# Performance work log

Hardware: AMD Instinct MI355X
Metric: run time of the kernel (lower is better)

The kernel has to match this reference:

```python
import jax, jax.numpy as jnp
import numpy as np

H, C = 2, 32  # heads, out_channels per head
NEG_SLOPE = 0.2


def gatv2_layer(h, src, dst, ea, W, b, We, att, bias, N):
    # shared lin_l = lin_r (share_weights=True)
    z = (h @ W + b).reshape(N, H, C)                      # [N,H,C]
    e = (ea @ We).reshape(-1, H, C)                        # [E',H,C]
    s = jax.nn.leaky_relu(z[dst] + z[src] + e, NEG_SLOPE)  # [E',H,C]
    alpha = jnp.einsum('ehc,hc->eh', s, att)               # [E',H]
    # segment softmax over destination neighborhoods
    m = jax.ops.segment_max(alpha, dst, num_segments=N)
    m = jnp.where(jnp.isfinite(m), m, 0.0)
    ex = jnp.exp(alpha - m[dst])
    denom = jax.ops.segment_sum(ex, dst, num_segments=N)
    a = ex / (denom[dst] + 1e-16)                          # [E',H]
    msg = (z[src] * a[:, :, None]).reshape(-1, H * C)      # [E',H*C]
    out = jax.ops.segment_sum(msg, dst, num_segments=N) + bias
    return out                                             # [N,H*C]


def setup_inputs() -> dict:
    key = jax.random.key(0)
    ks = jax.random.split(key, 16)
    N, E = 50000, 800000
    inp = {
        'x': jax.random.normal(ks[0], (N, 2), jnp.float32),
        'edge_index': jax.random.randint(ks[1], (2, E), 0, N, jnp.int64 if jax.config.jax_enable_x64 else jnp.int32).astype(jnp.int32),
        'edge_attr': jax.random.uniform(ks[2], (E, 2), jnp.float32),
        'dest_index': 123,
        'W0': jax.random.normal(ks[3], (2, 64), jnp.float32) * 0.5,
        'b0': jnp.zeros((64,), jnp.float32),
        'We0': jax.random.normal(ks[4], (2, 64), jnp.float32) * 0.5,
        'att0': jax.random.normal(ks[5], (H, C), jnp.float32) * 0.5,
        'bias0': jnp.zeros((64,), jnp.float32),
        'W1': jax.random.normal(ks[6], (64, 64), jnp.float32) * 0.125,
        'b1': jnp.zeros((64,), jnp.float32),
        'We1': jax.random.normal(ks[7], (2, 64), jnp.float32) * 0.5,
        'att1': jax.random.normal(ks[8], (H, C), jnp.float32) * 0.5,
        'bias1': jnp.zeros((64,), jnp.float32),
        'Wm1': jax.random.normal(ks[9], (194, 32), jnp.float32) * 0.07,
        'bm1': jnp.zeros((32,), jnp.float32),
        'Wm2': jax.random.normal(ks[10], (32, 1), jnp.float32) * 0.17,
        'bm2': jnp.zeros((1,), jnp.float32),
    }
    return inp


def reference(x, edge_index, edge_attr, dest_index,
              W0, b0, We0, att0, bias0,
              W1, b1, We1, att1, bias1,
              Wm1, bm1, Wm2, bm2):
    N = x.shape[0]
    # add self loops (fill_value='mean' for edge_attr)
    loops = jnp.arange(N, dtype=edge_index.dtype)
    src = jnp.concatenate([edge_index[0], loops])
    dst = jnp.concatenate([edge_index[1], loops])
    ea_sl = jnp.concatenate(
        [edge_attr, jnp.broadcast_to(edge_attr.mean(axis=0), (N, edge_attr.shape[1]))], axis=0)

    h = x
    h = jax.nn.elu(gatv2_layer(h, src, dst, ea_sl, W0, b0, We0, att0, bias0, N))
    h = jax.nn.elu(gatv2_layer(h, src, dst, ea_sl, W1, b1, We1, att1, bias1, N))

    goal = h[dest_index]                                   # [64]
    src_emb = h[edge_index[0]]                             # [E,64]
    dst_emb = h[edge_index[1]]                             # [E,64]
    goal_rep = jnp.broadcast_to(goal, (edge_index.shape[1], goal.shape[0]))
    edge_in = jnp.concatenate([src_emb, dst_emb, goal_rep, edge_attr], axis=-1)  # [E,194]
    hmlp = jax.nn.relu(edge_in @ Wm1 + bm1)
    logits = (hmlp @ Wm2 + bm2).squeeze(-1)                # [E]
    return logits
```

## Files before the change

kernel.cpp:

```cpp
#include <hip/hip_runtime.h>
#include <hip/hip_bf16.h>
#include <hip/hip_fp16.h>
#include <math.h>


typedef __attribute__((ext_vector_type(8))) short short8;
typedef __attribute__((ext_vector_type(4))) float f32x4;

#define BSH 6
#define CAP 2048
#define CH 4096

template <int IMM>
__device__ __forceinline__ float swz(float x) {
    return __int_as_float(__builtin_amdgcn_ds_swizzle(__float_as_int(x), IMM));
}

template <int CTRL>
__device__ __forceinline__ float dpp_add(float p) {
    int t = __builtin_amdgcn_update_dpp(0, __float_as_int(p), CTRL, 0xF, 0xF, true);
    return p + __int_as_float(t);
}

__device__ __forceinline__ short2 bsplit(float x) {
    unsigned u = __float_as_uint(x);
    short hi = (short)(u >> 16);
    float hif = __uint_as_float(u & 0xFFFF0000u);
    short lo = (short)(__float_as_uint(x - hif) >> 16);
    return make_short2(hi, lo);
}

__global__ __launch_bounds__(512) void setup_kernel(const float* __restrict__ W1,
                                                    const float* __restrict__ Wm1,
                                                    short* __restrict__ BfW1,
                                                    short* __restrict__ BfWm,
                                                    int* __restrict__ bucket_cursor,
                                                    float* __restrict__ easum, int nbuck) {
    if (blockIdx.x == 2) {
        for (int i = threadIdx.x; i < nbuck; i += 512) bucket_cursor[i] = i * CAP;
        if (threadIdx.x < 2) easum[threadIdx.x] = 0.f;
        return;
    }
    int snt = threadIdx.x >> 6;
    int lane = threadIdx.x & 63;
    int s = snt >> 2, nt = snt & 3;
    int col = nt * 16 + (lane & 15);
    short* Bf = blockIdx.x == 0 ? BfW1 : BfWm;
#pragma unroll
    for (int j = 0; j < 8; ++j) {
        int k = s * 32 + (lane >> 4) * 8 + j;
        float v;
        if (blockIdx.x == 0) {
            v = W1[k * 64 + col];
        } else {
            v = (col < 32) ? Wm1[k * 32 + col] : Wm1[(64 + k) * 32 + (col - 32)];
        }
        short2 t = bsplit(v);
        Bf[(snt * 2 + 0) * 512 + lane * 8 + j] = t.x;
        Bf[(snt * 2 + 1) * 512 + lane * 8 + j] = t.y;
    }
}

__global__ __launch_bounds__(256) void phaseA_kernel(const int* __restrict__ ei,
                                                     const float2* __restrict__ ea,
                                                     int* __restrict__ bucket_cursor,
                                                     float* __restrict__ easum,
                                                     float4* __restrict__ staged,
                                                     int E, int nbuck) {
    extern __shared__ int sm[];
    int* lcnt = sm;
    int* lbase = sm + nbuck;
    __shared__ float r0[4], r1[4];
    int tid = threadIdx.x;
    for (int i = tid; i < nbuck; i += 256) lcnt[i] = 0;
    __syncthreads();
    int base = blockIdx.x * CH;
    int end = min(base + CH, E);
    for (int i = base + tid; i < end; i += 256) {
        int d = ei[E + i];
        atomicAdd(&lcnt[d >> BSH], 1);
    }
    __syncthreads();
    for (int i = tid; i < nbuck; i += 256) {
        int c = lcnt[i];
        lbase[i] = c ? atomicAdd(&bucket_cursor[i], c) : 0;
        lcnt[i] = 0;
    }
    __syncthreads();
    float s0 = 0.f, s1 = 0.f;
    for (int i = base + tid; i < end; i += 256) {
        int s = ei[i], d = ei[E + i];
        float2 v = ea[i];
        s0 += v.x; s1 += v.y;
        int b = d >> BSH;
        int pos = lbase[b] + atomicAdd(&lcnt[b], 1);
        staged[pos] = make_float4(__int_as_float(s), v.x, v.y, __int_as_float(d));
    }
#pragma unroll
    for (int o = 32; o >= 1; o >>= 1) {
        s0 += __shfl_xor(s0, o);
        s1 += __shfl_xor(s1, o);
    }
    int wave = tid >> 6;
    if ((tid & 63) == 0) { r0[wave] = s0; r1[wave] = s1; }
    __syncthreads();
    if (tid == 0) {
        atomicAdd(&easum[0], r0[0] + r0[1] + r0[2] + r0[3]);
        atomicAdd(&easum[1], r1[0] + r1[1] + r1[2] + r1[3]);
    }
}

__global__ __launch_bounds__(512) void phaseB_mega(
    const float4* __restrict__ staged, const int* __restrict__ bucket_cursor,
    const float* __restrict__ easum, const float2* __restrict__ x,
    const float* __restrict__ W0, const float* __restrict__ b0,
    const float* __restrict__ We, const float* __restrict__ att,
    const float* __restrict__ bias, const short* __restrict__ Bf,
    const float* __restrict__ b1,
    int* __restrict__ row_ptr, float4* __restrict__ recs,
    __half* __restrict__ z16, int N, int E, int nbuck) {
    __shared__ int cnt64[64];
    __shared__ int offs[64];
    __shared__ int psum8[8];
    __shared__ float acc6[64][6];
    __shared__ float h0s[64 * 64];
    int b = blockIdx.x;
    int n0g = b << BSH;
    int tid = threadIdx.x;
    int lane = tid & 63;
    int wave = tid >> 6;
    int local = 0;
    for (int j = tid; j < b; j += 512) local += bucket_cursor[j] - j * CAP;
#pragma unroll
    for (int o = 32; o >= 1; o >>= 1) local += __shfl_xor(local, o);
    if (tid < 64) cnt64[tid] = 0;
    for (int i = tid; i < 64 * 6; i += 512) ((float*)acc6)[i] = 0.f;
    if (lane == 0) psum8[wave] = local;
    __syncthreads();
    int bbase = 64 * b + psum8[0] + psum8[1] + psum8[2] + psum8[3]
                       + psum8[4] + psum8[5] + psum8[6] + psum8[7];
    int sbeg = b * CAP;
    int send = bucket_cursor[b];
    int nsl = send - sbeg;
    int nodes_here = min(64, N - n0g);
    int nrec = nsl + nodes_here;
    float invE = 1.f / (float)E;
    float m0 = easum[0] * invE, m1 = easum[1] * invE;

    int m = lane & 15, quad = lane >> 4;
    {
        int c0 = quad * 8, c1 = 32 + c0;
        float w0a[8], w1a[8], ata[8], w0b[8], w1b[8], atb[8];
        float Wxa[8], Wya[8], bca[8], Wxb[8], Wyb[8], bcb[8];
#pragma unroll
        for (int j = 0; j < 8; ++j) {
            w0a[j] = We[c0 + j];  w1a[j] = We[64 + c0 + j];  ata[j] = att[c0 + j];
            w0b[j] = We[c1 + j];  w1b[j] = We[64 + c1 + j];  atb[j] = att[c1 + j];
            Wxa[j] = W0[c0 + j];  Wya[j] = W0[64 + c0 + j];  bca[j] = b0[c0 + j];
            Wxb[j] = W0[c1 + j];  Wyb[j] = W0[64 + c1 + j];  bcb[j] = b0[c1 + j];
        }
        int npass = (nsl + 15) >> 4;
        for (int p = wave; p < npass; p += 8) {
            int idx = p * 16 + m;
            bool valid = idx < nsl;
            float4 r = staged[sbeg + (valid ? idx : nsl - 1)];
            int s = __float_as_int(r.x);
            int d = __float_as_int(r.w);
            float2 xs = x[s];
            float2 xd = x[d];
            float P0 = 0.f, P1 = 0.f;
#pragma unroll
            for (int j = 0; j < 8; ++j) {
                float zs = fmaf(xs.x, Wxa[j], fmaf(xs.y, Wya[j], bca[j]));
                float zd = fmaf(xd.x, Wxa[j], fmaf(xd.y, Wya[j], bca[j]));
                float t0 = zd + zs + fmaf(r.y, w0a[j], r.z * w1a[j]);
                t0 = fmaxf(t0, 0.2f * t0);
                P0 = fmaf(t0, ata[j], P0);
                float zs1 = fmaf(xs.x, Wxb[j], fmaf(xs.y, Wyb[j], bcb[j]));
                float zd1 = fmaf(xd.x, Wxb[j], fmaf(xd.y, Wyb[j], bcb[j]));
                float t1 = zd1 + zs1 + fmaf(r.y, w0b[j], r.z * w1b[j]);
                t1 = fmaxf(t1, 0.2f * t1);
                P1 = fmaf(t1, atb[j], P1);
            }
            P0 += swz<0x401F>(P0);
            P1 += swz<0x401F>(P1);
            P0 += __shfl_xor(P0, 32);
            P1 += __shfl_xor(P1, 32);
            float w0 = __expf(fminf(P0, 60.f));
            float w1 = __expf(fminf(P1, 60.f));
            if (lane < 16 && valid) {
                int dl = d - n0g;
                atomicAdd(&acc6[dl][0], w0);
                atomicAdd(&acc6[dl][1], w0 * xs.x);
                atomicAdd(&acc6[dl][2], w0 * xs.y);
                atomicAdd(&acc6[dl][3], w1);
                atomicAdd(&acc6[dl][4], w1 * xs.x);
                atomicAdd(&acc6[dl][5], w1 * xs.y);
                atomicAdd(&cnt64[dl], 1);
            }
        }
    }
    __syncthreads();

    if (wave == 0) {
        int node = n0g + lane;
        int tot = cnt64[lane] + ((node < N) ? 1 : 0);
        int v = tot;
#pragma unroll
        for (int st = 1; st < 64; st <<= 1) {
            int u = __shfl_up(v, st);
            if (lane >= st) v += u;
        }
        if (node < N) {
            int excl = bbase + v - tot;
            row_ptr[node] = excl;
            recs[excl] = make_float4(__int_as_float(node), m0, m1, __int_as_float(node));
            offs[lane] = excl + 1;
        }
        if (b == nbuck - 1 && lane == 0) row_ptr[N] = bbase + nrec;
    }
    for (int k = 0; k < 8; ++k) {
        int q = wave + 8 * k;
        int ch = lane;
        int node = n0g + q;
        float hv = 0.f;
        if (node < N) {
            float2 xn = x[node];
            float W0c = W0[ch], W0c2 = W0[64 + ch], b0c = b0[ch];
            float zn = fmaf(xn.x, W0c, fmaf(xn.y, W0c2, b0c));
            float ts = fmaf(2.f, zn, fmaf(m0, We[ch], m1 * We[64 + ch]));
            ts = fmaxf(ts, 0.2f * ts);
            float p = ts * att[ch];
#pragma unroll
            for (int o = 1; o <= 16; o <<= 1) p += __shfl_xor(p, o);
            float wself = __expf(fminf(p, 60.f));
            int hsel = (ch >= 32) ? 3 : 0;
            float l  = acc6[q][hsel]     + wself;
            float Sx = acc6[q][hsel + 1] + wself * xn.x;
            float Sy = acc6[q][hsel + 2] + wself * xn.y;
            float num = fmaf(W0c, Sx, fmaf(W0c2, Sy, b0c * l));
            float v = num / (l + 1e-16f) + bias[ch];
            hv = (v > 0.f) ? v : expm1f(v);
        }
        h0s[q * 64 + ch] = hv;
    }
    __syncthreads();

    if (wave < 4) {
        int rowb = wave * 16 + m;
        f32x4 acc[4] = {{0.f, 0.f, 0.f, 0.f}, {0.f, 0.f, 0.f, 0.f},
                        {0.f, 0.f, 0.f, 0.f}, {0.f, 0.f, 0.f, 0.f}};
#pragma unroll
        for (int s = 0; s < 2; ++s) {
            const float* ap = h0s + rowb * 64 + s * 32 + quad * 8;
            float4 a0 = *(const float4*)ap;
            float4 a1 = *(const float4*)(ap + 4);
            short8 ahi, alo;
            short2 t;
            t = bsplit(a0.x); ahi[0] = t.x; alo[0] = t.y;
            t = bsplit(a0.y); ahi[1] = t.x; alo[1] = t.y;
            t = bsplit(a0.z); ahi[2] = t.x; alo[2] = t.y;
            t = bsplit(a0.w); ahi[3] = t.x; alo[3] = t.y;
            t = bsplit(a1.x); ahi[4] = t.x; alo[4] = t.y;
            t = bsplit(a1.y); ahi[5] = t.x; alo[5] = t.y;
            t = bsplit(a1.z); ahi[6] = t.x; alo[6] = t.y;
            t = bsplit(a1.w); ahi[7] = t.x; alo[7] = t.y;
#pragma unroll
            for (int nt = 0; nt < 4; ++nt) {
                const short* bp = Bf + ((s * 4 + nt) * 2) * 512 + lane * 8;
                short8 bhi = *(const short8*)bp;
                short8 blo = *(const short8*)(bp + 512);
                acc[nt] = __builtin_amdgcn_mfma_f32_16x16x32_bf16(ahi, bhi, acc[nt], 0, 0, 0);
                acc[nt] = __builtin_amdgcn_mfma_f32_16x16x32_bf16(ahi, blo, acc[nt], 0, 0, 0);
                acc[nt] = __builtin_amdgcn_mfma_f32_16x16x32_bf16(alo, bhi, acc[nt], 0, 0, 0);
            }
        }
#pragma unroll
        for (int nt = 0; nt < 4; ++nt) {
            int col = nt * 16 + m;
            float bj = b1[col];
#pragma unroll
            for (int r = 0; r < 4; ++r) {
                int orow = n0g + wave * 16 + quad * 4 + r;
                if (orow < N) z16[(size_t)orow * 64 + col] = __float2half(acc[nt][r] + bj);
            }
        }
    } else {
        for (int i = sbeg + (tid - 256); i < send; i += 256) {
            float4 r = staged[i];
            int d = __float_as_int(r.w);
            int pos = atomicAdd(&offs[d - n0g], 1);
            recs[pos] = r;
        }
    }
}

__global__ __launch_bounds__(256) void agg1_kernel(
    const __half* __restrict__ z, const int* __restrict__ row_ptr,
    const float4* __restrict__ recs,
    const float* __restrict__ We, const float* __restrict__ att,
    const float* __restrict__ bias, float* __restrict__ hout, int N) {
    int gtid = blockIdx.x * blockDim.x + threadIdx.x;
    int n = gtid >> 6;
    if (n >= N) return;
    n = __builtin_amdgcn_readfirstlane(n);
    int lane = threadIdx.x & 63;
    int half = lane >> 5;
    int c = (lane & 31) * 2;

    float We0a = We[c],      We0b = We[c + 1];
    float We1a = We[64 + c], We1b = We[64 + c + 1];
    float atta = att[c],     attb = att[c + 1];
    float2 znf = __half22float2(*(const __half2*)(z + (size_t)n * 64 + c));

    int beg = row_ptr[n], end = row_ptr[n + 1];
    float ll[4] = {0.f, 0.f, 0.f, 0.f};
    float a0[4] = {0.f, 0.f, 0.f, 0.f};
    float a1[4] = {0.f, 0.f, 0.f, 0.f};
    for (int i = beg; i < end; i += 8) {
        float w[4]; float2 zs[4];
#pragma unroll
        for (int k = 0; k < 4; ++k) {
            int idx = i + 2 * k + half;
            int idc = idx < end ? idx : end - 1;
            float4 r = recs[idc];
            int s = __float_as_int(r.x);
            zs[k] = __half22float2(*(const __half2*)(z + (size_t)s * 64 + c));
            float sj0 = znf.x + zs[k].x + fmaf(r.y, We0a, r.z * We1a);
            float sj1 = znf.y + zs[k].y + fmaf(r.y, We0b, r.z * We1b);
            sj0 = fmaxf(sj0, 0.2f * sj0);
            sj1 = fmaxf(sj1, 0.2f * sj1);
            float p = fmaf(sj0, atta, sj1 * attb);
            p = dpp_add<0xB1>(p);
            p = dpp_add<0x4E>(p);
            p = dpp_add<0x141>(p);
            p = dpp_add<0x140>(p);
            float ww = __expf(fminf(p, 60.f));
            w[k] = (idx < end) ? ww : 0.f;
        }
#pragma unroll
        for (int k = 0; k < 4; ++k) {
            ll[k] += w[k];
            a0[k] = fmaf(w[k], zs[k].x, a0[k]);
            a1[k] = fmaf(w[k], zs[k].y, a1[k]);
        }
    }
    float l  = (ll[0] + ll[1]) + (ll[2] + ll[3]);
    float s0 = (a0[0] + a0[1]) + (a0[2] + a0[3]);
    float s1 = (a1[0] + a1[1]) + (a1[2] + a1[3]);
    l  += __shfl_xor(l, 32);
    s0 += __shfl_xor(s0, 32);
    s1 += __shfl_xor(s1, 32);
    float inv = 1.f / (l + 1e-16f);
    float v0 = s0 * inv + bias[c];
    float v1 = s1 * inv + bias[c + 1];
    v0 = (v0 > 0.f) ? v0 : expm1f(v0);
    v1 = (v1 > 0.f) ? v1 : expm1f(v1);
    *(float2*)(hout + (size_t)n * 64 + c) = make_float2(v0, v1);
}

__global__ __launch_bounds__(256) void mfma_gemm64(const float* __restrict__ h,
                                                   const short* __restrict__ Bf,
                                                   __half* __restrict__ out, int N,
                                                   const float* __restrict__ Wm1,
                                                   const float* __restrict__ bm1,
                                                   const int* __restrict__ dest,
                                                   float* __restrict__ gv) {
    int wave = threadIdx.x >> 6;
    int lane = threadIdx.x & 63;
    int n0 = blockIdx.x * 64 + wave * 16;
    if (n0 < N) {
        int m = lane & 15, quad = lane >> 4;
        int arow = n0 + m;
        if (arow > N - 1) arow = N - 1;
        f32x4 acc[4] = {{0.f, 0.f, 0.f, 0.f}, {0.f, 0.f, 0.f, 0.f},
                        {0.f, 0.f, 0.f, 0.f}, {0.f, 0.f, 0.f, 0.f}};
#pragma unroll
        for (int s = 0; s < 2; ++s) {
            const float* ap = h + (size_t)arow * 64 + s * 32 + quad * 8;
            float4 a0 = *(const float4*)ap;
            float4 a1 = *(const float4*)(ap + 4);
            short8 ahi, alo;
            short2 t;
            t = bsplit(a0.x); ahi[0] = t.x; alo[0] = t.y;
            t = bsplit(a0.y); ahi[1] = t.x; alo[1] = t.y;
            t = bsplit(a0.z); ahi[2] = t.x; alo[2] = t.y;
            t = bsplit(a0.w); ahi[3] = t.x; alo[3] = t.y;
            t = bsplit(a1.x); ahi[4] = t.x; alo[4] = t.y;
            t = bsplit(a1.y); ahi[5] = t.x; alo[5] = t.y;
            t = bsplit(a1.z); ahi[6] = t.x; alo[6] = t.y;
            t = bsplit(a1.w); ahi[7] = t.x; alo[7] = t.y;
#pragma unroll
            for (int nt = 0; nt < 4; ++nt) {
                const short* bp = Bf + ((s * 4 + nt) * 2) * 512 + lane * 8;
                short8 bhi = *(const short8*)bp;
                short8 blo = *(const short8*)(bp + 512);
                acc[nt] = __builtin_amdgcn_mfma_f32_16x16x32_bf16(ahi, bhi, acc[nt], 0, 0, 0);
                acc[nt] = __builtin_amdgcn_mfma_f32_16x16x32_bf16(ahi, blo, acc[nt], 0, 0, 0);
                acc[nt] = __builtin_amdgcn_mfma_f32_16x16x32_bf16(alo, bhi, acc[nt], 0, 0, 0);
            }
        }
#pragma unroll
        for (int nt = 0; nt < 4; ++nt) {
            int col = nt * 16 + m;
#pragma unroll
            for (int r = 0; r < 4; ++r) {
                int orow = n0 + quad * 4 + r;
                if (orow < N) out[(size_t)orow * 64 + col] = __float2half(acc[nt][r]);
            }
        }
    }
    if (gv && blockIdx.x == 0 && threadIdx.x < 32) {
        int dd = dest[0];
        int q = threadIdx.x;
        float acc2 = bm1[q];
        for (int k = 0; k < 64; ++k)
            acc2 = fmaf(h[(size_t)dd * 64 + k], Wm1[(128 + k) * 32 + q], acc2);
        gv[q] = acc2;
    }
}

__global__ __launch_bounds__(256) void edge_mlp_kernel(
    const int* __restrict__ ei, const float2* __restrict__ ea,
    const __half* __restrict__ hsd, const float* __restrict__ gvec,
    const float* __restrict__ WrowA, const float* __restrict__ WrowB,
    const float* __restrict__ Wm2, const float* __restrict__ bm2,
    float* __restrict__ out, int E) {
    int tid = blockIdx.x * blockDim.x + threadIdx.x;
    int e = tid >> 3;
    int j = tid & 7;
    if (e >= E) return;
    int s = ei[e], d = ei[E + e];
    float2 eav = ea[e];
    const __half2* ps = (const __half2*)(hsd + (size_t)s * 64 + j * 4);
    const __half2* pd = (const __half2*)(hsd + (size_t)d * 64 + 32 + j * 4);
    float2 a01 = __half22float2(ps[0]), a23 = __half22float2(ps[1]);
    float2 b01 = __half22float2(pd[0]), b23 = __half22float2(pd[1]);
    float4 g = *(const float4*)(gvec + j * 4);
    float4 wa = *(const float4*)(WrowA + j * 4);
    float4 wb = *(const float4*)(WrowB + j * 4);
    float4 w2 = *(const float4*)(Wm2 + j * 4);
    float acc = 0.f, v;
    v = fmaf(eav.x, wa.x, fmaf(eav.y, wb.x, a01.x + b01.x + g.x)); v = fmaxf(v, 0.f); acc = fmaf(v, w2.x, acc);
    v = fmaf(eav.x, wa.y, fmaf(eav.y, wb.y, a01.y + b01.y + g.y)); v = fmaxf(v, 0.f); acc = fmaf(v, w2.y, acc);
    v = fmaf(eav.x, wa.z, fmaf(eav.y, wb.z, a23.x + b23.x + g.z)); v = fmaxf(v, 0.f); acc = fmaf(v, w2.z, acc);
    v = fmaf(eav.x, wa.w, fmaf(eav.y, wb.w, a23.y + b23.y + g.w)); v = fmaxf(v, 0.f); acc = fmaf(v, w2.w, acc);
    acc = dpp_add<0xB1>(acc);
    acc = dpp_add<0x4E>(acc);
    acc = dpp_add<0x141>(acc);
    if (j == 0) out[e] = acc + bm2[0];
}

extern "C" void kernel_launch(void* const* d_in, const int* in_sizes, int n_in,
                              void* d_out, int out_size, void* d_ws, size_t ws_size,
                              hipStream_t stream) {
    const float* x     = (const float*)d_in[0];
    const int*   ei    = (const int*)d_in[1];
    const float* ea    = (const float*)d_in[2];
    const int*   dest  = (const int*)d_in[3];
    const float* W0    = (const float*)d_in[4];
    const float* b0    = (const float*)d_in[5];
    const float* We0   = (const float*)d_in[6];
    const float* att0  = (const float*)d_in[7];
    const float* bias0 = (const float*)d_in[8];
    const float* W1    = (const float*)d_in[9];
    const float* b1    = (const float*)d_in[10];
    const float* We1   = (const float*)d_in[11];
    const float* att1  = (const float*)d_in[12];
    const float* bias1 = (const float*)d_in[13];
    const float* Wm1   = (const float*)d_in[14];
    const float* bm1   = (const float*)d_in[15];
    const float* Wm2   = (const float*)d_in[16];
    const float* bm2   = (const float*)d_in[17];

    const int N = in_sizes[0] / 2;
    const int E = in_sizes[1] / 2;
    const int nbuck = (N + 63) >> BSH;
    const int nchunk = (E + CH - 1) / CH;

    char* ws = (char*)d_ws;
    size_t off = 0;
    auto alloc = [&](size_t bytes) -> void* {
        void* p = ws + off;
        off += bytes;
        off = (off + 255) & ~(size_t)255;
        return p;
    };
    int*    bucket_cursor = (int*)alloc((size_t)nbuck * 4);
    int*    row_ptr       = (int*)alloc((size_t)(N + 1) * 4);
    size_t  slack_bytes   = (size_t)nbuck * CAP * 16;
    float4* staged        = (float4*)alloc(slack_bytes);
    float4* recs          = (float4*)alloc((size_t)(E + N) * 16);
    __half* z16           = (__half*)alloc((size_t)N * 64 * 2);
    float*  hbuf          = (float*)alloc((size_t)N * 64 * 4);
    float*  easum         = (float*)alloc(8);
    float*  gvec          = (float*)alloc(32 * 4);
    short*  BfW1          = (short*)alloc(8192 * 2);
    short*  BfWm          = (short*)alloc(8192 * 2);
    __half* hsd16         = z16;

    dim3 blk(256);
    setup_kernel<<<3, 512, 0, stream>>>(W1, Wm1, BfW1, BfWm, bucket_cursor, easum, nbuck);
    phaseA_kernel<<<nchunk, blk, (size_t)nbuck * 8, stream>>>(ei, (const float2*)ea,
                                                              bucket_cursor, easum,
                                                              staged, E, nbuck);
    phaseB_mega<<<nbuck, 512, 0, stream>>>(staged, bucket_cursor, easum,
                                           (const float2*)x, W0, b0, We0, att0, bias0,
                                           BfW1, b1, row_ptr, recs, z16, N, E, nbuck);
    agg1_kernel<<<(N * 64 + 255) / 256, blk, 0, stream>>>(z16, row_ptr, recs,
                                                          We1, att1, bias1, hbuf, N);
    mfma_gemm64<<<(N + 63) / 64, blk, 0, stream>>>(hbuf, BfWm, hsd16, N,
                                                   Wm1, bm1, dest, gvec);
    edge_mlp_kernel<<<((size_t)E * 8 + 255) / 256, blk, 0, stream>>>(
        ei, (const float2*)ea, hsd16, gvec,
        Wm1 + 192 * 32, Wm1 + 193 * 32, Wm2, bm2, (float*)d_out, E);
}
```

Measured before the change: 272.1 us.

## Rebalance phaseB work mapping: 4 channels/lane edge scoring, split MFMA across all waves

The edge-scoring loop now maps 16 lanes per edge with 4 channels each, so a wave handles 4 edges per pass instead of 16 lanes × 16 channels. This lowers register pressure, and a swizzle tree reduction replaces the earlier cross-half shuffles. The layer-1 MFMA transform is now split across all 8 waves (2 column tiles each) rather than 4, and all 512 threads then scatter records. Launch bounds add a min-blocks hint of 8 to raise occupancy. The trade-offs are more loop passes and extra per-edge gather and atomic traffic in the scoring loop, plus possible spills under the tighter register limit.

```diff
diff --git a/kernel.cpp b/kernel.cpp
--- a/kernel.cpp
+++ b/kernel.cpp
@@ -110,7 +110,7 @@
     }
 }
 
-__global__ __launch_bounds__(512) void phaseB_mega(
+__global__ __launch_bounds__(512, 8) void phaseB_mega(
     const float4* __restrict__ staged, const int* __restrict__ bucket_cursor,
     const float* __restrict__ easum, const float2* __restrict__ x,
     const float* __restrict__ W0, const float* __restrict__ b0,
@@ -147,48 +147,43 @@
     float invE = 1.f / (float)E;
     float m0 = easum[0] * invE, m1 = easum[1] * invE;
 
-    int m = lane & 15, quad = lane >> 4;
     {
-        int c0 = quad * 8, c1 = 32 + c0;
-        float w0a[8], w1a[8], ata[8], w0b[8], w1b[8], atb[8];
-        float Wxa[8], Wya[8], bca[8], Wxb[8], Wyb[8], bcb[8];
-#pragma unroll
-        for (int j = 0; j < 8; ++j) {
-            w0a[j] = We[c0 + j];  w1a[j] = We[64 + c0 + j];  ata[j] = att[c0 + j];
-            w0b[j] = We[c1 + j];  w1b[j] = We[64 + c1 + j];  atb[j] = att[c1 + j];
-            Wxa[j] = W0[c0 + j];  Wya[j] = W0[64 + c0 + j];  bca[j] = b0[c0 + j];
-            Wxb[j] = W0[c1 + j];  Wyb[j] = W0[64 + c1 + j];  bcb[j] = b0[c1 + j];
-        }
-        int npass = (nsl + 15) >> 4;
+        int sub = lane & 15;
+        int eslot = lane >> 4;
+        int ch0 = ((sub & 7) << 2) + ((sub >> 3) << 5);
+        float Wx[4], Wy[4], bc[4], w0e[4], w1e[4], at[4];
+#pragma unroll
+        for (int j = 0; j < 4; ++j) {
+            Wx[j] = W0[ch0 + j];  Wy[j] = W0[64 + ch0 + j];  bc[j] = b0[ch0 + j];
+            w0e[j] = We[ch0 + j]; w1e[j] = We[64 + ch0 + j]; at[j] = att[ch0 + j];
+        }
+        int npass = (nsl + 3) >> 2;
         for (int p = wave; p < npass; p += 8) {
-            int idx = p * 16 + m;
+            int idx = p * 4 + eslot;
             bool valid = idx < nsl;
             float4 r = staged[sbeg + (valid ? idx : nsl - 1)];
             int s = __float_as_int(r.x);
             int d = __float_as_int(r.w);
             float2 xs = x[s];
             float2 xd = x[d];
-            float P0 = 0.f, P1 = 0.f;
-#pragma unroll
-            for (int j = 0; j < 8; ++j) {
-                float zs = fmaf(xs.x, Wxa[j], fmaf(xs.y, Wya[j], bca[j]));
-                float zd = fmaf(xd.x, Wxa[j], fmaf(xd.y, Wya[j], bca[j]));
-                float t0 = zd + zs + fmaf(r.y, w0a[j], r.z * w1a[j]);
+            float P = 0.f;
+#pragma unroll
+            for (int j = 0; j < 4; ++j) {
+                float zs = fmaf(xs.x, Wx[j], fmaf(xs.y, Wy[j], bc[j]));
+                float zd = fmaf(xd.x, Wx[j], fmaf(xd.y, Wy[j], bc[j]));
+                float t0 = zd + zs + fmaf(r.y, w0e[j], r.z * w1e[j]);
                 t0 = fmaxf(t0, 0.2f * t0);
-                P0 = fmaf(t0, ata[j], P0);
-                float zs1 = fmaf(xs.x, Wxb[j], fmaf(xs.y, Wyb[j], bcb[j]));
-                float zd1 = fmaf(xd.x, Wxb[j], fmaf(xd.y, Wyb[j], bcb[j]));
-                float t1 = zd1 + zs1 + fmaf(r.y, w0b[j], r.z * w1b[j]);
-                t1 = fmaxf(t1, 0.2f * t1);
-                P1 = fmaf(t1, atb[j], P1);
+                P = fmaf(t0, at[j], P);
             }
-            P0 += swz<0x401F>(P0);
-            P1 += swz<0x401F>(P1);
-            P0 += __shfl_xor(P0, 32);
-            P1 += __shfl_xor(P1, 32);
-            float w0 = __expf(fminf(P0, 60.f));
-            float w1 = __expf(fminf(P1, 60.f));
-            if (lane < 16 && valid) {
+            P += swz<0x041F>(P);
+            P += swz<0x081F>(P);
+            P += swz<0x101F>(P);
+            float Po = swz<0x201F>(P);
+            float Ph0 = (sub < 8) ? P : Po;
+            float Ph1 = (sub < 8) ? Po : P;
+            float w0 = __expf(fminf(Ph0, 60.f));
+            float w1 = __expf(fminf(Ph1, 60.f));
+            if (sub == 0 && valid) {
                 int dl = d - n0g;
                 atomicAdd(&acc6[dl][0], w0);
                 atomicAdd(&acc6[dl][1], w0 * xs.x);
@@ -246,52 +241,50 @@
     }
     __syncthreads();
 
-    if (wave < 4) {
-        int rowb = wave * 16 + m;
-        f32x4 acc[4] = {{0.f, 0.f, 0.f, 0.f}, {0.f, 0.f, 0.f, 0.f},
-                        {0.f, 0.f, 0.f, 0.f}, {0.f, 0.f, 0.f, 0.f}};
-#pragma unroll
-        for (int s = 0; s < 2; ++s) {
-            const float* ap = h0s + rowb * 64 + s * 32 + quad * 8;
-            float4 a0 = *(const float4*)ap;
-            float4 a1 = *(const float4*)(ap + 4);
-            short8 ahi, alo;
-            short2 t;
-            t = bsplit(a0.x); ahi[0] = t.x; alo[0] = t.y;
-            t = bsplit(a0.y); ahi[1] = t.x; alo[1] = t.y;
-            t = bsplit(a0.z); ahi[2] = t.x; alo[2] = t.y;
-            t = bsplit(a0.w); ahi[3] = t.x; alo[3] = t.y;
-            t = bsplit(a1.x); ahi[4] = t.x; alo[4] = t.y;
-            t = bsplit(a1.y); ahi[5] = t.x; alo[5] = t.y;
-            t = bsplit(a1.z); ahi[6] = t.x; alo[6] = t.y;
-            t = bsplit(a1.w); ahi[7] = t.x; alo[7] = t.y;
-#pragma unroll
-            for (int nt = 0; nt < 4; ++nt) {
-                const short* bp = Bf + ((s * 4 + nt) * 2) * 512 + lane * 8;
-                short8 bhi = *(const short8*)bp;
-                short8 blo = *(const short8*)(bp + 512);
-                acc[nt] = __builtin_amdgcn_mfma_f32_16x16x32_bf16(ahi, bhi, acc[nt], 0, 0, 0);
-                acc[nt] = __builtin_amdgcn_mfma_f32_16x16x32_bf16(ahi, blo, acc[nt], 0, 0, 0);
-                acc[nt] = __builtin_amdgcn_mfma_f32_16x16x32_bf16(alo, bhi, acc[nt], 0, 0, 0);
-            }
-        }
-#pragma unroll
-        for (int nt = 0; nt < 4; ++nt) {
-            int col = nt * 16 + m;
-            float bj = b1[col];
-#pragma unroll
-            for (int r = 0; r < 4; ++r) {
-                int orow = n0g + wave * 16 + quad * 4 + r;
-                if (orow < N) z16[(size_t)orow * 64 + col] = __float2half(acc[nt][r] + bj);
-            }
-        }
-    } else {
-        for (int i = sbeg + (tid - 256); i < send; i += 256) {
-            float4 r = staged[i];
-            int d = __float_as_int(r.w);
-            int pos = atomicAdd(&offs[d - n0g], 1);
-            recs[pos] = r;
-        }
+    int m = lane & 15, quad = lane >> 4;
+    int rowb = (wave & 3) * 16 + m;
+    int ntb = (wave >> 2) * 2;
+    f32x4 acc[2] = {{0.f, 0.f, 0.f, 0.f}, {0.f, 0.f, 0.f, 0.f}};
+#pragma unroll
+    for (int s = 0; s < 2; ++s) {
+        const float* ap = h0s + rowb * 64 + s * 32 + quad * 8;
+        float4 a0 = *(const float4*)ap;
+        float4 a1 = *(const float4*)(ap + 4);
+        short8 ahi, alo;
+        short2 t;
+        t = bsplit(a0.x); ahi[0] = t.x; alo[0] = t.y;
+        t = bsplit(a0.y); ahi[1] = t.x; alo[1] = t.y;
+        t = bsplit(a0.z); ahi[2] = t.x; alo[2] = t.y;
+        t = bsplit(a0.w); ahi[3] = t.x; alo[3] = t.y;
+        t = bsplit(a1.x); ahi[4] = t.x; alo[4] = t.y;
+        t = bsplit(a1.y); ahi[5] = t.x; alo[5] = t.y;
+        t = bsplit(a1.z); ahi[6] = t.x; alo[6] = t.y;
+        t = bsplit(a1.w); ahi[7] = t.x; alo[7] = t.y;
+#pragma unroll
+        for (int u = 0; u < 2; ++u) {
+            const short* bp = Bf + ((s * 4 + ntb + u) * 2) * 512 + lane * 8;
+            short8 bhi = *(const short8*)bp;
+            short8 blo = *(const short8*)(bp + 512);
+            acc[u] = __builtin_amdgcn_mfma_f32_16x16x32_bf16(ahi, bhi, acc[u], 0, 0, 0);
+            acc[u] = __builtin_amdgcn_mfma_f32_16x16x32_bf16(ahi, blo, acc[u], 0, 0, 0);
+            acc[u] = __builtin_amdgcn_mfma_f32_16x16x32_bf16(alo, bhi, acc[u], 0, 0, 0);
+        }
+    }
+#pragma unroll
+    for (int u = 0; u < 2; ++u) {
+        int col = (ntb + u) * 16 + m;
+        float bj = b1[col];
+#pragma unroll
+        for (int r = 0; r < 4; ++r) {
+            int orow = n0g + (wave & 3) * 16 + quad * 4 + r;
+            if (orow < N) z16[(size_t)orow * 64 + col] = __float2half(acc[u][r] + bj);
+        }
+    }
+    for (int i = sbeg + tid; i < send; i += 512) {
+        float4 r = staged[i];
+        int d = __float_as_int(r.w);
+        int pos = atomicAdd(&offs[d - n0g], 1);
+        recs[pos] = r;
     }
 }
 
```

After: 255.8 us. -6.0%, faster.
